# Optimization experiments

Measured on AMD Instinct MI355X. Metric: run time of the kernel, lower is better.

## Reference

```python
import jax, jax.numpy as jnp
import numpy as np

N_QUBITS = 10
INPUT_DIM = 49
ENC_LAMBDA = float(np.pi)
ENC_BETA_MAX = 1.0
BATCH = 2048
LOGIT_SCALE_MIN, LOGIT_SCALE_MAX = 0.5, 80.0
LOGIT_CLAMP = 30.0

# arch_mat rows: [control, target, op, axis, feature]; op: ENC=1, ROT=2, CNOT=3; 1-indexed, 0=none.
def _build_arch_mat():
    cols = []
    for b in range(3):
        for q in range(N_QUBITS):  # encoding RY gates
            cols.append((0, q + 1, 1, 2, (b * N_QUBITS + q) % INPUT_DIM + 1))
        for q in range(N_QUBITS):  # trainable RX gates
            cols.append((0, q + 1, 2, 1, 0))
        for q in range(N_QUBITS - 1):  # CNOT chain
            cols.append((q + 1, q + 2, 3, 0, 0))
    return np.asarray(cols, dtype=np.int64).T  # (5, L)

ARCH_MAT = _build_arch_mat()
N_THETA = int(((ARCH_MAT[2] == 2) & (ARCH_MAT[1] > 0) & (ARCH_MAT[3] > 0)).sum())


def _apply_rot(state, ax, q, theta):
    # state: (B, 2,...,2) complex64; theta: scalar or (B,)
    st = jnp.moveaxis(state, 1 + q, -1)
    half = 0.5 * theta
    c, s = jnp.cos(half), jnp.sin(half)
    if c.ndim == 1:  # per-sample angle -> broadcast over remaining qubit axes
        shape = (-1,) + (1,) * (st.ndim - 2)
        c, s = c.reshape(shape), s.reshape(shape)
    s0, s1 = st[..., 0], st[..., 1]
    if ax == 1:  # RX
        n0 = c * s0 - 1j * s * s1
        n1 = c * s1 - 1j * s * s0
    elif ax == 2:  # RY
        n0 = c * s0 - s * s1
        n1 = c * s1 + s * s0
    else:  # RZ
        n0 = (c - 1j * s) * s0
        n1 = (c + 1j * s) * s1
    return jnp.moveaxis(jnp.stack([n0, n1], axis=-1), -1, 1 + q)


def _apply_cnot(state, cq, tq):
    st = jnp.moveaxis(state, (1 + cq, 1 + tq), (-2, -1))
    st = jnp.stack([st[..., 0, :], st[..., 1, ::-1]], axis=-2)
    return jnp.moveaxis(st, (-2, -1), (1 + cq, 1 + tq))


def _circuit(x, theta, enc_alpha_raw, enc_beta_raw):
    B = x.shape[0]
    state = jnp.zeros((B,) + (2,) * N_QUBITS, jnp.complex64)
    state = state.at[(slice(None),) + (0,) * N_QUBITS].set(1.0)
    alpha = jax.nn.softplus(enc_alpha_raw) + 1e-6  # (D,)
    beta = jnp.tanh(enc_beta_raw) * ENC_BETA_MAX   # (D,)
    rot_idx = 0
    for l in range(ARCH_MAT.shape[1]):  # static structural loop over gates
        c, t, op, ax, f1 = (int(v) for v in ARCH_MAT[:, l])
        if op == 1 and t > 0 and ax > 0 and f1 > 0:
            fi = f1 - 1
            ang = ENC_LAMBDA * (alpha[fi] * x[:, fi] + beta[fi])  # (B,)
            state = _apply_rot(state, ax, t - 1, ang)
        elif op == 2 and t > 0 and ax > 0:
            state = _apply_rot(state, ax, t - 1, theta[rot_idx])
            rot_idx += 1
        elif op == 3 and c > 0 and t > 0 and c != t:
            state = _apply_cnot(state, c - 1, t - 1)
    probs = state.real ** 2 + state.imag ** 2  # (B, 2,...,2)
    exps = []
    for q in range(N_QUBITS):  # <Z_q> = p(q=0) - p(q=1)
        p = jnp.moveaxis(probs, 1 + q, -1).reshape(B, -1, 2).sum(axis=1)
        exps.append(p[:, 0] - p[:, 1])
    return jnp.stack(exps, axis=1)  # (B, n_qubits)


def setup_inputs() -> dict:
    key = jax.random.key(0)
    k = jax.random.split(key, 4)
    x = jax.random.normal(k[0], (BATCH, INPUT_DIM), jnp.float32)
    theta = jnp.clip(0.01 * jax.random.normal(k[1], (N_THETA,), jnp.float32), -0.1, 0.1)
    a0 = float(np.log(np.exp(1.0) - 1.0))  # softplus^-1(enc_alpha_init=1.0)
    enc_alpha_raw = jnp.full((INPUT_DIM,), a0, jnp.float32)
    enc_beta_raw = jnp.zeros((INPUT_DIM,), jnp.float32)  # arctanh(0)=0
    head_w = 0.02 * jax.random.normal(k[2], (1, N_QUBITS), jnp.float32)
    bound = 1.0 / float(np.sqrt(N_QUBITS))
    head_b = jax.random.uniform(k[3], (1,), jnp.float32, -bound, bound)
    logit_scale = jnp.asarray(1.0, jnp.float32)
    return {"x": x, "theta": theta, "enc_alpha_raw": enc_alpha_raw, "enc_beta_raw": enc_beta_raw,
            "head_w": head_w, "head_b": head_b, "logit_scale": logit_scale}


def reference(x, theta, enc_alpha_raw, enc_beta_raw, head_w, head_b, logit_scale):
    exps = _circuit(x, theta, enc_alpha_raw, enc_beta_raw)  # (B, n_qubits)
    raw = exps @ head_w.T + head_b                          # (B, 1)
    scale = jnp.clip(logit_scale, LOGIT_SCALE_MIN, LOGIT_SCALE_MAX)
    return jnp.clip(scale * raw, -LOGIT_CLAMP, LOGIT_CLAMP)
```

## Files before the change

### kernel.cpp

```cpp
#include <hip/hip_runtime.h>
#include <math.h>


#define PI_F 3.14159265358979323846f

typedef unsigned v2u __attribute__((ext_vector_type(2)));

#if defined(__has_builtin)
#if __has_builtin(__builtin_amdgcn_permlane16_swap)
#define HAVE_PL16 1
#endif
#if __has_builtin(__builtin_amdgcn_permlane32_swap)
#define HAVE_PL32 1
#endif
#endif

__device__ __forceinline__ float rdlane(float v, int l) {
    return __int_as_float(__builtin_amdgcn_readlane(__float_as_int(v), l));
}

__device__ __forceinline__ float xor1p(float v) {
    return __int_as_float(__builtin_amdgcn_update_dpp(
        0, __float_as_int(v), 0xB1, 0xF, 0xF, true));
}
__device__ __forceinline__ float xor2p(float v) {
    return __int_as_float(__builtin_amdgcn_update_dpp(
        0, __float_as_int(v), 0x4E, 0xF, 0xF, true));
}
__device__ __forceinline__ float xor4p(float v) {
    int t = __builtin_amdgcn_update_dpp(0, __float_as_int(v), 0x1B, 0xF, 0xF, true);
    t = __builtin_amdgcn_update_dpp(0, t, 0x141, 0xF, 0xF, true);
    return __int_as_float(t);
}
__device__ __forceinline__ float xor8p(float v) {
    return __int_as_float(__builtin_amdgcn_update_dpp(
        0, __float_as_int(v), 0x128, 0xF, 0xF, true));
}
__device__ __forceinline__ float xor16p(float v, bool hi) {
#ifdef HAVE_PL16
    v2u r = __builtin_amdgcn_permlane16_swap(
        (unsigned)__float_as_int(v), (unsigned)__float_as_int(v), false, false);
    return __int_as_float((int)(hi ? r.x : r.y));
#else
    return __shfl_xor(v, 16);
#endif
}
__device__ __forceinline__ float xor32p(float v, bool hi) {
#ifdef HAVE_PL32
    v2u r = __builtin_amdgcn_permlane32_swap(
        (unsigned)__float_as_int(v), (unsigned)__float_as_int(v), false, false);
    return __int_as_float((int)(hi ? r.x : r.y));
#else
    return __shfl_xor(v, 32);
#endif
}

template<int Q>
__device__ __forceinline__ float lane_xor(float v, bool hi) {
    if constexpr (Q == 0) return xor1p(v);
    else if constexpr (Q == 1) return xor2p(v);
    else if constexpr (Q == 2) return xor4p(v);
    else if constexpr (Q == 3) return xor8p(v);
    else if constexpr (Q == 4) return xor16p(v, hi);
    else return xor32p(v, hi);
}

template<bool NEG>
__device__ __forceinline__ float2 cgate(const float2 ar2, const float2 ai2,
                                        const float2 br2, const float2 bi2,
                                        const float2 v, const float2 w) {
    float2 acc;
    asm("v_pk_mul_f32 %0, %1, %2" : "=v"(acc) : "v"(ar2), "v"(v));
    if constexpr (!NEG) {
        asm("v_pk_fma_f32 %0, %1, %2, %0 op_sel:[0,1,0] op_sel_hi:[1,0,1] neg_lo:[0,1,0]"
            : "+v"(acc) : "v"(ai2), "v"(v));
        asm("v_pk_fma_f32 %0, %1, %2, %0" : "+v"(acc) : "v"(br2), "v"(w));
    } else {
        asm("v_pk_fma_f32 %0, %1, %2, %0 op_sel:[0,1,0] op_sel_hi:[1,0,1] neg_lo:[1,1,0] neg_hi:[1,0,0]"
            : "+v"(acc) : "v"(ai2), "v"(v));
        asm("v_pk_fma_f32 %0, %1, %2, %0 neg_lo:[1,0,0] neg_hi:[1,0,0]"
            : "+v"(acc) : "v"(br2), "v"(w));
    }
    asm("v_pk_fma_f32 %0, %1, %2, %0 op_sel:[0,1,0] op_sel_hi:[1,0,1] neg_lo:[0,1,0]"
        : "+v"(acc) : "v"(bi2), "v"(w));
    return acc;
}

template<int Q>
__device__ __forceinline__ void lane_gate(float2 (&st)[8], int lane,
                                          float ar, float ai, float br, float bi) {
    const bool hi = (lane & (1 << Q)) != 0;
    const float aiL = hi ? -ai : ai;
    const float brL = hi ? -br : br;
    const float2 ar2 = make_float2(ar, ar);
    const float2 ai2 = make_float2(aiL, aiL);
    const float2 br2 = make_float2(brL, brL);
    const float2 bi2 = make_float2(bi, bi);
    #pragma unroll
    for (int r = 0; r < 8; ++r) {
        float2 p;
        p.x = lane_xor<Q>(st[r].x, hi);
        p.y = lane_xor<Q>(st[r].y, hi);
        st[r] = cgate<false>(ar2, ai2, br2, bi2, st[r], p);
    }
}

template<int RB>
__device__ __forceinline__ void reg_gate(float2 (&st)[8],
                                         float ar, float ai, float br, float bi) {
    const float2 ar2 = make_float2(ar, ar);
    const float2 ai2 = make_float2(ai, ai);
    const float2 br2 = make_float2(br, br);
    const float2 bi2 = make_float2(bi, bi);
    #pragma unroll
    for (int r = 0; r < 8; ++r) {
        if ((r & RB) == 0) {
            const int r1 = r | RB;
            const float2 v0 = st[r], v1 = st[r1];
            st[r]  = cgate<false>(ar2, ai2, br2, bi2, v0, v1);
            st[r1] = cgate<true >(ar2, ai2, br2, bi2, v1, v0);
        }
    }
}

__global__ __launch_bounds__(128, 4) void cqv_kernel(
    const float* __restrict__ x,
    const float* __restrict__ theta,
    const float* __restrict__ alpha_raw,
    const float* __restrict__ beta_raw,
    const float* __restrict__ head_w,
    const float* __restrict__ head_b,
    const float* __restrict__ logit_scale,
    float* __restrict__ out,
    int batch)
{
    const int lane = threadIdx.x & 63;
    const int wv = threadIdx.x >> 6;
    const int s = blockIdx.x;

    __shared__ float2 lds[2][8][2][64];
    __shared__ float pbuf[2];

    const int l5 = (lane >> 5) & 1;
    const int srcLane = lane ^ ((lane & 31) << 1);

    const int g = (lane < 30) ? lane : 0;
    const float alpha = log1pf(__expf(alpha_raw[g])) + 1e-6f;
    const float beta  = tanhf(beta_raw[g]);
    const float halfE = 0.5f * PI_F * (alpha * x[s * 49 + g] + beta);
    float cE, sE, cT, sT;
    __sincosf(halfE, &sE, &cE);
    __sincosf(0.5f * theta[g], &sT, &cT);

    float2 st[8];

    {
        float u0r[10], u0i[10], u1r[10], u1i[10];
        #pragma unroll
        for (int q = 0; q < 10; ++q) {
            const float ce = rdlane(cE, q), se = rdlane(sE, q);
            const float ct = rdlane(cT, q), s_t = rdlane(sT, q);
            u0r[q] = ct * ce;  u0i[q] = -s_t * se;
            u1r[q] = ct * se;  u1i[q] = -s_t * ce;
        }
        float plr = 1.f, pli = 0.f;
        #pragma unroll
        for (int q = 0; q < 6; ++q) {
            const bool bq = (lane >> q) & 1;
            const float wr = bq ? u1r[q] : u0r[q];
            const float wi = bq ? u1i[q] : u0i[q];
            const float nr = plr * wr - pli * wi;
            const float ni = plr * wi + pli * wr;
            plr = nr; pli = ni;
        }
        const float w9r = wv ? u1r[9] : u0r[9], w9i = wv ? u1i[9] : u0i[9];
        float t67r[4], t67i[4], t89r[2], t89i[2];
        #pragma unroll
        for (int a = 0; a < 4; ++a) {
            const float w6r = (a & 1) ? u1r[6] : u0r[6], w6i = (a & 1) ? u1i[6] : u0i[6];
            const float w7r = (a & 2) ? u1r[7] : u0r[7], w7i = (a & 2) ? u1i[7] : u0i[7];
            t67r[a] = w6r * w7r - w6i * w7i;  t67i[a] = w6r * w7i + w6i * w7r;
        }
        #pragma unroll
        for (int k = 0; k < 2; ++k) {
            const float w8r = k ? u1r[8] : u0r[8], w8i = k ? u1i[8] : u0i[8];
            t89r[k] = w8r * w9r - w8i * w9i;  t89i[k] = w8r * w9i + w8i * w9r;
        }
        #pragma unroll
        for (int r = 0; r < 8; ++r) {
            const float ar = t67r[r & 3] * t89r[r >> 2] - t67i[r & 3] * t89i[r >> 2];
            const float ai = t67r[r & 3] * t89i[r >> 2] + t67i[r & 3] * t89r[r >> 2];
            st[r].x = ar * plr - ai * pli;
            st[r].y = ar * pli + ai * plr;
        }
    }

    {
        #pragma unroll
        for (int r = 0; r < 8; ++r) lds[0][r][wv][lane] = st[r];
        __syncthreads();
        #pragma unroll
        for (int r = 0; r < 8; ++r) {
            const int sReg = (r ^ ((r & 3) << 1)) ^ l5;
            const int k9 = wv ^ (r >> 2);
            st[r] = lds[0][sReg][k9][srcLane];
        }
    }

#define GATE_PARAMS(BASE, Q) \
        const float ce = rdlane(cE, (BASE) + (Q)), se = rdlane(sE, (BASE) + (Q)); \
        const float ct = rdlane(cT, (BASE) + (Q)), s_t = rdlane(sT, (BASE) + (Q));
#define APPLY_LANE_GATE(BASE, Q) { GATE_PARAMS(BASE, Q) \
        lane_gate<Q>(st, lane, ct * ce, -s_t * se, -ct * se, -s_t * ce); }
#define APPLY_REG_GATE(BASE, Q, RB) { GATE_PARAMS(BASE, Q) \
        reg_gate<RB>(st, ct * ce, -s_t * se, -ct * se, -s_t * ce); }
#define APPLY_Q0_Q8(BASE) \
        APPLY_LANE_GATE(BASE, 0) APPLY_LANE_GATE(BASE, 1) APPLY_LANE_GATE(BASE, 2) \
        APPLY_LANE_GATE(BASE, 3) APPLY_LANE_GATE(BASE, 4) APPLY_LANE_GATE(BASE, 5) \
        APPLY_REG_GATE(BASE, 6, 1) APPLY_REG_GATE(BASE, 7, 2) APPLY_REG_GATE(BASE, 8, 4)

    {
        APPLY_Q0_Q8(10)
        GATE_PARAMS(10, 9)
        const float ar = ct * ce, ai = -s_t * se, br = -ct * se, bi = -s_t * ce;
        const float2 ar2 = make_float2(ar, ar), ai2 = make_float2(ai, ai);
        const float2 br2 = make_float2(br, br), bi2 = make_float2(bi, bi);
        #pragma unroll
        for (int r = 0; r < 8; ++r) lds[1][r][wv][lane] = st[r];
        __syncthreads();
        #pragma unroll
        for (int r = 0; r < 8; ++r) {
            const int sReg = (r ^ ((r & 3) << 1)) ^ l5;
            const int k9 = wv ^ (r >> 2);
            const float2 v = lds[1][sReg][k9][srcLane];
            const float2 w = lds[1][sReg][k9 ^ 1][srcLane];
            if (k9 == 0) st[r] = cgate<false>(ar2, ai2, br2, bi2, v, w);
            else         st[r] = cgate<true >(ar2, ai2, br2, bi2, v, w);
        }
    }

    {
        APPLY_Q0_Q8(20)
        GATE_PARAMS(20, 9)
        const float ar = ct * ce, ai = -s_t * se, br = -ct * se, bi = -s_t * ce;
        const float2 ar2 = make_float2(ar, ar), ai2 = make_float2(ai, ai);
        const float2 br2 = make_float2(br, br), bi2 = make_float2(bi, bi);
        #pragma unroll
        for (int r = 0; r < 8; ++r) lds[0][r][wv][lane] = st[r];
        __syncthreads();
        #pragma unroll
        for (int r = 0; r < 8; ++r) {
            const float2 w = lds[0][r][wv ^ 1][lane];
            if (wv == 0) st[r] = cgate<false>(ar2, ai2, br2, bi2, st[r], w);
            else         st[r] = cgate<true >(ar2, ai2, br2, bi2, st[r], w);
        }
    }
#undef GATE_PARAMS
#undef APPLY_LANE_GATE
#undef APPLY_REG_GATE
#undef APPLY_Q0_Q8

    float w[10];
    #pragma unroll
    for (int q = 0; q < 10; ++q) w[q] = head_w[q];
    float wlane = 0.f;
    {
        int pref = 0;
        #pragma unroll
        for (int q = 0; q < 6; ++q) {
            pref ^= (lane >> q) & 1;
            wlane += pref ? -w[q] : w[q];
        }
    }
    const float sPL = ((__builtin_popcount(lane & 63) & 1) ? -1.f : 1.f);
    float acc = 0.f, psum = 0.f;
    #pragma unroll
    for (int r = 0; r < 8; ++r) {
        const float pw = st[r].x * st[r].x + st[r].y * st[r].y;
        const int p0 = r & 1, p1 = p0 ^ ((r >> 1) & 1), p2 = p1 ^ ((r >> 2) & 1);
        const float wr = (p0 ? -w[6] : w[6]) + (p1 ? -w[7] : w[7])
                       + (p2 ? -w[8] : w[8]) + ((p2 ^ wv) ? -w[9] : w[9]);
        psum += pw;
        acc = fmaf(wr, pw, acc);
    }
    float partial = fmaf(wlane, psum, sPL * acc);
    #pragma unroll
    for (int off = 32; off >= 1; off >>= 1) partial += __shfl_xor(partial, off);

    if (lane == 0) pbuf[wv] = partial;
    __syncthreads();
    if (threadIdx.x == 0) {
        const float scale = fminf(fmaxf(logit_scale[0], 0.5f), 80.f);
        const float raw = pbuf[0] + pbuf[1] + head_b[0];
        out[s] = fminf(fmaxf(scale * raw, -30.f), 30.f);
    }
}

extern "C" void kernel_launch(void* const* d_in, const int* in_sizes, int n_in,
                              void* d_out, int out_size, void* d_ws, size_t ws_size,
                              hipStream_t stream) {
    const int B = in_sizes[0] / 49;
    dim3 block(128);
    dim3 grid(B);
    cqv_kernel<<<grid, block, 0, stream>>>(
        (const float*)d_in[0], (const float*)d_in[1], (const float*)d_in[2],
        (const float*)d_in[3], (const float*)d_in[4], (const float*)d_in[5],
        (const float*)d_in[6], (float*)d_out, B);
}
```

Baseline: 79.74 us.

## Split each 1024-amplitude state across four waves instead of two

Each sample's state vector is now spread over four wavefronts (256 threads), each holding 4 amplitudes per lane instead of 8. Qubits 8 and 9 both become wave-index qubits. Their gates are applied together through one LDS exchange that reads four partner values per element, and the CNOT permutation is folded into the LDS addressing. The aim is to halve per-thread serial gate work and register pressure and to raise occupancy, at the cost of more LDS traffic, redundant per-wave parameter setup and a larger reduction.

Result: slower. 84.44 us (+5.9%).

```diff
diff --git a/kernel.cpp b/kernel.cpp
--- a/kernel.cpp
+++ b/kernel.cpp
@@ -17,6 +17,9 @@
 
 __device__ __forceinline__ float rdlane(float v, int l) {
     return __int_as_float(__builtin_amdgcn_readlane(__float_as_int(v), l));
+}
+__device__ __forceinline__ float rdfirst(float v) {
+    return __int_as_float(__builtin_amdgcn_readfirstlane(__float_as_int(v)));
 }
 
 __device__ __forceinline__ float xor1p(float v) {
@@ -65,65 +68,105 @@
     else return xor32p(v, hi);
 }
 
+struct CG { float2 ar2, ai2, br2, bi2; };
+__device__ __forceinline__ CG mkcg(float ce, float se, float ct, float s_t) {
+    const float ar = ct * ce, ai = -s_t * se, br = -ct * se, bi = -s_t * ce;
+    CG g;
+    g.ar2 = make_float2(ar, ar); g.ai2 = make_float2(ai, ai);
+    g.br2 = make_float2(br, br); g.bi2 = make_float2(bi, bi);
+    return g;
+}
+
 template<bool NEG>
-__device__ __forceinline__ float2 cgate(const float2 ar2, const float2 ai2,
-                                        const float2 br2, const float2 bi2,
-                                        const float2 v, const float2 w) {
+__device__ __forceinline__ float2 cgate(const CG& g, const float2 v, const float2 w) {
     float2 acc;
-    asm("v_pk_mul_f32 %0, %1, %2" : "=v"(acc) : "v"(ar2), "v"(v));
+    asm("v_pk_mul_f32 %0, %1, %2" : "=v"(acc) : "v"(g.ar2), "v"(v));
     if constexpr (!NEG) {
         asm("v_pk_fma_f32 %0, %1, %2, %0 op_sel:[0,1,0] op_sel_hi:[1,0,1] neg_lo:[0,1,0]"
-            : "+v"(acc) : "v"(ai2), "v"(v));
-        asm("v_pk_fma_f32 %0, %1, %2, %0" : "+v"(acc) : "v"(br2), "v"(w));
+            : "+v"(acc) : "v"(g.ai2), "v"(v));
+        asm("v_pk_fma_f32 %0, %1, %2, %0" : "+v"(acc) : "v"(g.br2), "v"(w));
     } else {
         asm("v_pk_fma_f32 %0, %1, %2, %0 op_sel:[0,1,0] op_sel_hi:[1,0,1] neg_lo:[1,1,0] neg_hi:[1,0,0]"
-            : "+v"(acc) : "v"(ai2), "v"(v));
+            : "+v"(acc) : "v"(g.ai2), "v"(v));
         asm("v_pk_fma_f32 %0, %1, %2, %0 neg_lo:[1,0,0] neg_hi:[1,0,0]"
-            : "+v"(acc) : "v"(br2), "v"(w));
+            : "+v"(acc) : "v"(g.br2), "v"(w));
     }
     asm("v_pk_fma_f32 %0, %1, %2, %0 op_sel:[0,1,0] op_sel_hi:[1,0,1] neg_lo:[0,1,0]"
-        : "+v"(acc) : "v"(bi2), "v"(w));
+        : "+v"(acc) : "v"(g.bi2), "v"(w));
     return acc;
 }
 
 template<int Q>
-__device__ __forceinline__ void lane_gate(float2 (&st)[8], int lane,
+__device__ __forceinline__ void lane_gate(float2 (&st)[4], int lane,
                                           float ar, float ai, float br, float bi) {
     const bool hi = (lane & (1 << Q)) != 0;
     const float aiL = hi ? -ai : ai;
     const float brL = hi ? -br : br;
-    const float2 ar2 = make_float2(ar, ar);
-    const float2 ai2 = make_float2(aiL, aiL);
-    const float2 br2 = make_float2(brL, brL);
-    const float2 bi2 = make_float2(bi, bi);
-    #pragma unroll
-    for (int r = 0; r < 8; ++r) {
+    CG g;
+    g.ar2 = make_float2(ar, ar);  g.ai2 = make_float2(aiL, aiL);
+    g.br2 = make_float2(brL, brL); g.bi2 = make_float2(bi, bi);
+    #pragma unroll
+    for (int r = 0; r < 4; ++r) {
         float2 p;
         p.x = lane_xor<Q>(st[r].x, hi);
         p.y = lane_xor<Q>(st[r].y, hi);
-        st[r] = cgate<false>(ar2, ai2, br2, bi2, st[r], p);
+        st[r] = cgate<false>(g, st[r], p);
     }
 }
 
 template<int RB>
-__device__ __forceinline__ void reg_gate(float2 (&st)[8],
-                                         float ar, float ai, float br, float bi) {
-    const float2 ar2 = make_float2(ar, ar);
-    const float2 ai2 = make_float2(ai, ai);
-    const float2 br2 = make_float2(br, br);
-    const float2 bi2 = make_float2(bi, bi);
-    #pragma unroll
-    for (int r = 0; r < 8; ++r) {
+__device__ __forceinline__ void reg_gate(float2 (&st)[4], const CG& g) {
+    #pragma unroll
+    for (int r = 0; r < 4; ++r) {
         if ((r & RB) == 0) {
             const int r1 = r | RB;
             const float2 v0 = st[r], v1 = st[r1];
-            st[r]  = cgate<false>(ar2, ai2, br2, bi2, v0, v1);
-            st[r1] = cgate<true >(ar2, ai2, br2, bi2, v1, v0);
-        }
-    }
-}
-
-__global__ __launch_bounds__(128, 4) void cqv_kernel(
+            st[r]  = cgate<false>(g, v0, v1);
+            st[r1] = cgate<true >(g, v1, v0);
+        }
+    }
+}
+
+template<int K8, int K9>
+__device__ __forceinline__ void exch_chain(float2 (&st)[4],
+                                           float2 (&buf)[4][4][64],
+                                           int l5, int srcLane,
+                                           const CG& g8, const CG& g9) {
+    #pragma unroll
+    for (int r = 0; r < 4; ++r) {
+        const int r0 = r & 1, r1 = r >> 1;
+        const int sReg = (r0 ^ l5) | ((r1 ^ r0) << 1);
+        const float2 s00 = buf[sReg][0][srcLane];
+        const float2 s01 = buf[sReg][1][srcLane];
+        const float2 s10 = buf[sReg][2][srcLane];
+        const float2 s11 = buf[sReg][3][srcLane];
+        float2 t0, t1;
+        if ((K8 ^ r1) == 0) { t0 = cgate<false>(g8, s00, s01); t1 = cgate<false>(g8, s10, s11); }
+        else                { t0 = cgate<true >(g8, s01, s00); t1 = cgate<true >(g8, s11, s10); }
+        if ((K9 ^ K8) == 0) st[r] = cgate<false>(g9, t0, t1);
+        else                st[r] = cgate<true >(g9, t1, t0);
+    }
+}
+
+template<int K8, int K9>
+__device__ __forceinline__ void exch_final(float2 (&st)[4],
+                                           float2 (&buf)[4][4][64],
+                                           int lane, const CG& g8, const CG& g9) {
+    #pragma unroll
+    for (int r = 0; r < 4; ++r) {
+        const float2 s00 = buf[r][0][lane];
+        const float2 s01 = buf[r][1][lane];
+        const float2 s10 = buf[r][2][lane];
+        const float2 s11 = buf[r][3][lane];
+        float2 t0, t1;
+        if (K8 == 0) { t0 = cgate<false>(g8, s00, s01); t1 = cgate<false>(g8, s10, s11); }
+        else         { t0 = cgate<true >(g8, s01, s00); t1 = cgate<true >(g8, s11, s10); }
+        if (K9 == 0) st[r] = cgate<false>(g9, t0, t1);
+        else         st[r] = cgate<true >(g9, t1, t0);
+    }
+}
+
+__global__ __launch_bounds__(256, 8) void cqv_kernel(
     const float* __restrict__ x,
     const float* __restrict__ theta,
     const float* __restrict__ alpha_raw,
@@ -137,12 +180,14 @@
     const int lane = threadIdx.x & 63;
     const int wv = threadIdx.x >> 6;
     const int s = blockIdx.x;
-
-    __shared__ float2 lds[2][8][2][64];
-    __shared__ float pbuf[2];
+    if (s >= batch) return;
+
+    __shared__ float2 lds[2][4][4][64];
+    __shared__ float pbuf[4];
 
     const int l5 = (lane >> 5) & 1;
     const int srcLane = lane ^ ((lane & 31) << 1);
+    const int k8 = wv & 1, k9 = (wv >> 1) & 1;
 
     const int g = (lane < 30) ? lane : 0;
     const float alpha = log1pf(__expf(alpha_raw[g])) + 1e-6f;
@@ -152,117 +197,116 @@
     __sincosf(halfE, &sE, &cE);
     __sincosf(0.5f * theta[g], &sT, &cT);
 
-    float2 st[8];
-
-    {
-        float u0r[10], u0i[10], u1r[10], u1i[10];
-        #pragma unroll
-        for (int q = 0; q < 10; ++q) {
+    float2 st[4];
+
+    {
+        float plr = 1.f, pli = 0.f;
+        #pragma unroll
+        for (int q = 0; q < 6; ++q) {
             const float ce = rdlane(cE, q), se = rdlane(sE, q);
             const float ct = rdlane(cT, q), s_t = rdlane(sT, q);
-            u0r[q] = ct * ce;  u0i[q] = -s_t * se;
-            u1r[q] = ct * se;  u1i[q] = -s_t * ce;
-        }
-        float plr = 1.f, pli = 0.f;
-        #pragma unroll
-        for (int q = 0; q < 6; ++q) {
             const bool bq = (lane >> q) & 1;
-            const float wr = bq ? u1r[q] : u0r[q];
-            const float wi = bq ? u1i[q] : u0i[q];
-            const float nr = plr * wr - pli * wi;
-            const float ni = plr * wi + pli * wr;
+            const float fr = bq ? ct * se : ct * ce;
+            const float fi = bq ? -s_t * ce : -s_t * se;
+            const float nr = plr * fr - pli * fi;
+            const float ni = plr * fi + pli * fr;
             plr = nr; pli = ni;
         }
-        const float w9r = wv ? u1r[9] : u0r[9], w9i = wv ? u1i[9] : u0i[9];
-        float t67r[4], t67i[4], t89r[2], t89i[2];
-        #pragma unroll
-        for (int a = 0; a < 4; ++a) {
-            const float w6r = (a & 1) ? u1r[6] : u0r[6], w6i = (a & 1) ? u1i[6] : u0i[6];
-            const float w7r = (a & 2) ? u1r[7] : u0r[7], w7i = (a & 2) ? u1i[7] : u0i[7];
-            t67r[a] = w6r * w7r - w6i * w7i;  t67i[a] = w6r * w7i + w6i * w7r;
-        }
-        #pragma unroll
-        for (int k = 0; k < 2; ++k) {
-            const float w8r = k ? u1r[8] : u0r[8], w8i = k ? u1i[8] : u0i[8];
-            t89r[k] = w8r * w9r - w8i * w9i;  t89i[k] = w8r * w9i + w8i * w9r;
-        }
-        #pragma unroll
-        for (int r = 0; r < 8; ++r) {
-            const float ar = t67r[r & 3] * t89r[r >> 2] - t67i[r & 3] * t89i[r >> 2];
-            const float ai = t67r[r & 3] * t89i[r >> 2] + t67i[r & 3] * t89r[r >> 2];
-            st[r].x = ar * plr - ai * pli;
-            st[r].y = ar * pli + ai * plr;
-        }
-    }
-
-    {
-        #pragma unroll
-        for (int r = 0; r < 8; ++r) lds[0][r][wv][lane] = st[r];
+        {
+            const float ce = rdlane(cE, 8), se = rdlane(sE, 8);
+            const float ct = rdlane(cT, 8), s_t = rdlane(sT, 8);
+            const float fr = k8 ? ct * se : ct * ce;
+            const float fi = k8 ? -s_t * ce : -s_t * se;
+            const float nr = plr * fr - pli * fi, ni = plr * fi + pli * fr;
+            plr = nr; pli = ni;
+        }
+        {
+            const float ce = rdlane(cE, 9), se = rdlane(sE, 9);
+            const float ct = rdlane(cT, 9), s_t = rdlane(sT, 9);
+            const float fr = k9 ? ct * se : ct * ce;
+            const float fi = k9 ? -s_t * ce : -s_t * se;
+            const float nr = plr * fr - pli * fi, ni = plr * fi + pli * fr;
+            plr = nr; pli = ni;
+        }
+        const float c6 = rdlane(cE, 6), s6 = rdlane(sE, 6);
+        const float ct6 = rdlane(cT, 6), st6 = rdlane(sT, 6);
+        const float c7 = rdlane(cE, 7), s7 = rdlane(sE, 7);
+        const float ct7 = rdlane(cT, 7), st7 = rdlane(sT, 7);
+        #pragma unroll
+        for (int r = 0; r < 4; ++r) {
+            const float f6r = (r & 1) ? ct6 * s6 : ct6 * c6;
+            const float f6i = (r & 1) ? -st6 * c6 : -st6 * s6;
+            const float f7r = (r & 2) ? ct7 * s7 : ct7 * c7;
+            const float f7i = (r & 2) ? -st7 * c7 : -st7 * s7;
+            const float tr_ = f6r * f7r - f6i * f7i;
+            const float ti_ = f6r * f7i + f6i * f7r;
+            st[r].x = tr_ * plr - ti_ * pli;
+            st[r].y = tr_ * pli + ti_ * plr;
+        }
+    }
+
+    {
+        #pragma unroll
+        for (int r = 0; r < 4; ++r) lds[0][r][wv][lane] = st[r];
         __syncthreads();
         #pragma unroll
-        for (int r = 0; r < 8; ++r) {
-            const int sReg = (r ^ ((r & 3) << 1)) ^ l5;
-            const int k9 = wv ^ (r >> 2);
-            st[r] = lds[0][sReg][k9][srcLane];
-        }
-    }
-
-#define GATE_PARAMS(BASE, Q) \
-        const float ce = rdlane(cE, (BASE) + (Q)), se = rdlane(sE, (BASE) + (Q)); \
-        const float ct = rdlane(cT, (BASE) + (Q)), s_t = rdlane(sT, (BASE) + (Q));
-#define APPLY_LANE_GATE(BASE, Q) { GATE_PARAMS(BASE, Q) \
+        for (int r = 0; r < 4; ++r) {
+            const int r0 = r & 1, r1 = r >> 1;
+            const int sReg = (r0 ^ l5) | ((r1 ^ r0) << 1);
+            const int sW = (k8 ^ r1) | ((k9 ^ k8) << 1);
+            st[r] = lds[0][sReg][sW][srcLane];
+        }
+    }
+
+#define GATE_PARAMS(GI) \
+        const float ce = rdlane(cE, (GI)), se = rdlane(sE, (GI)); \
+        const float ct = rdlane(cT, (GI)), s_t = rdlane(sT, (GI));
+#define APPLY_LANE_GATE(BASE, Q) { GATE_PARAMS((BASE) + (Q)) \
         lane_gate<Q>(st, lane, ct * ce, -s_t * se, -ct * se, -s_t * ce); }
-#define APPLY_REG_GATE(BASE, Q, RB) { GATE_PARAMS(BASE, Q) \
-        reg_gate<RB>(st, ct * ce, -s_t * se, -ct * se, -s_t * ce); }
-#define APPLY_Q0_Q8(BASE) \
+#define APPLY_REG_GATE(BASE, Q, RB) { GATE_PARAMS((BASE) + (Q)) \
+        reg_gate<RB>(st, mkcg(ce, se, ct, s_t)); }
+#define APPLY_Q0_Q7(BASE) \
         APPLY_LANE_GATE(BASE, 0) APPLY_LANE_GATE(BASE, 1) APPLY_LANE_GATE(BASE, 2) \
         APPLY_LANE_GATE(BASE, 3) APPLY_LANE_GATE(BASE, 4) APPLY_LANE_GATE(BASE, 5) \
-        APPLY_REG_GATE(BASE, 6, 1) APPLY_REG_GATE(BASE, 7, 2) APPLY_REG_GATE(BASE, 8, 4)
-
-    {
-        APPLY_Q0_Q8(10)
-        GATE_PARAMS(10, 9)
-        const float ar = ct * ce, ai = -s_t * se, br = -ct * se, bi = -s_t * ce;
-        const float2 ar2 = make_float2(ar, ar), ai2 = make_float2(ai, ai);
-        const float2 br2 = make_float2(br, br), bi2 = make_float2(bi, bi);
-        #pragma unroll
-        for (int r = 0; r < 8; ++r) lds[1][r][wv][lane] = st[r];
+        APPLY_REG_GATE(BASE, 6, 1) APPLY_REG_GATE(BASE, 7, 2)
+
+    {
+        APPLY_Q0_Q7(10)
+        const CG g8 = mkcg(rdlane(cE, 18), rdlane(sE, 18), rdlane(cT, 18), rdlane(sT, 18));
+        const CG g9 = mkcg(rdlane(cE, 19), rdlane(sE, 19), rdlane(cT, 19), rdlane(sT, 19));
+        #pragma unroll
+        for (int r = 0; r < 4; ++r) lds[1][r][wv][lane] = st[r];
         __syncthreads();
-        #pragma unroll
-        for (int r = 0; r < 8; ++r) {
-            const int sReg = (r ^ ((r & 3) << 1)) ^ l5;
-            const int k9 = wv ^ (r >> 2);
-            const float2 v = lds[1][sReg][k9][srcLane];
-            const float2 w = lds[1][sReg][k9 ^ 1][srcLane];
-            if (k9 == 0) st[r] = cgate<false>(ar2, ai2, br2, bi2, v, w);
-            else         st[r] = cgate<true >(ar2, ai2, br2, bi2, v, w);
-        }
-    }
-
-    {
-        APPLY_Q0_Q8(20)
-        GATE_PARAMS(20, 9)
-        const float ar = ct * ce, ai = -s_t * se, br = -ct * se, bi = -s_t * ce;
-        const float2 ar2 = make_float2(ar, ar), ai2 = make_float2(ai, ai);
-        const float2 br2 = make_float2(br, br), bi2 = make_float2(bi, bi);
-        #pragma unroll
-        for (int r = 0; r < 8; ++r) lds[0][r][wv][lane] = st[r];
+        switch (wv) {
+            case 0:  exch_chain<0, 0>(st, lds[1], l5, srcLane, g8, g9); break;
+            case 1:  exch_chain<1, 0>(st, lds[1], l5, srcLane, g8, g9); break;
+            case 2:  exch_chain<0, 1>(st, lds[1], l5, srcLane, g8, g9); break;
+            default: exch_chain<1, 1>(st, lds[1], l5, srcLane, g8, g9); break;
+        }
+    }
+
+    {
+        APPLY_Q0_Q7(20)
+        const CG g8 = mkcg(rdlane(cE, 28), rdlane(sE, 28), rdlane(cT, 28), rdlane(sT, 28));
+        const CG g9 = mkcg(rdlane(cE, 29), rdlane(sE, 29), rdlane(cT, 29), rdlane(sT, 29));
+        #pragma unroll
+        for (int r = 0; r < 4; ++r) lds[0][r][wv][lane] = st[r];
         __syncthreads();
-        #pragma unroll
-        for (int r = 0; r < 8; ++r) {
-            const float2 w = lds[0][r][wv ^ 1][lane];
-            if (wv == 0) st[r] = cgate<false>(ar2, ai2, br2, bi2, st[r], w);
-            else         st[r] = cgate<true >(ar2, ai2, br2, bi2, st[r], w);
+        switch (wv) {
+            case 0:  exch_final<0, 0>(st, lds[0], lane, g8, g9); break;
+            case 1:  exch_final<1, 0>(st, lds[0], lane, g8, g9); break;
+            case 2:  exch_final<0, 1>(st, lds[0], lane, g8, g9); break;
+            default: exch_final<1, 1>(st, lds[0], lane, g8, g9); break;
         }
     }
 #undef GATE_PARAMS
 #undef APPLY_LANE_GATE
 #undef APPLY_REG_GATE
-#undef APPLY_Q0_Q8
+#undef APPLY_Q0_Q7
 
     float w[10];
     #pragma unroll
-    for (int q = 0; q < 10; ++q) w[q] = head_w[q];
+    for (int q = 0; q < 10; ++q) w[q] = rdfirst(head_w[q]);
     float wlane = 0.f;
     {
         int pref = 0;
@@ -272,14 +316,14 @@
             wlane += pref ? -w[q] : w[q];
         }
     }
-    const float sPL = ((__builtin_popcount(lane & 63) & 1) ? -1.f : 1.f);
+    const float sPL = (__builtin_popcount(lane & 63) & 1) ? -1.f : 1.f;
     float acc = 0.f, psum = 0.f;
     #pragma unroll
-    for (int r = 0; r < 8; ++r) {
+    for (int r = 0; r < 4; ++r) {
         const float pw = st[r].x * st[r].x + st[r].y * st[r].y;
-        const int p0 = r & 1, p1 = p0 ^ ((r >> 1) & 1), p2 = p1 ^ ((r >> 2) & 1);
+        const int p0 = r & 1, p1 = p0 ^ (r >> 1);
         const float wr = (p0 ? -w[6] : w[6]) + (p1 ? -w[7] : w[7])
-                       + (p2 ? -w[8] : w[8]) + ((p2 ^ wv) ? -w[9] : w[9]);
+                       + ((p1 ^ k8) ? -w[8] : w[8]) + ((p1 ^ k8 ^ k9) ? -w[9] : w[9]);
         psum += pw;
         acc = fmaf(wr, pw, acc);
     }
@@ -291,7 +335,7 @@
     __syncthreads();
     if (threadIdx.x == 0) {
         const float scale = fminf(fmaxf(logit_scale[0], 0.5f), 80.f);
-        const float raw = pbuf[0] + pbuf[1] + head_b[0];
+        const float raw = pbuf[0] + pbuf[1] + pbuf[2] + pbuf[3] + head_b[0];
         out[s] = fminf(fmaxf(scale * raw, -30.f), 30.f);
     }
 }
@@ -300,7 +344,7 @@
                               void* d_out, int out_size, void* d_ws, size_t ws_size,
                               hipStream_t stream) {
     const int B = in_sizes[0] / 49;
-    dim3 block(128);
+    dim3 block(256);
     dim3 grid(B);
     cqv_kernel<<<grid, block, 0, stream>>>(
         (const float*)d_in[0], (const float*)d_in[1], (const float*)d_in[2],
```
